# Kernel optimization log

Hardware: AMD Instinct MI355X
Metric: run time of the kernel (lower is better)

Reference implementation:

```python
import jax, jax.numpy as jnp
import numpy as np

BS, L, D, K, G, E = 512, 128, 512, 30, 8, 2048
H = E // 2  # MLP hidden = embed_dim // 2


def setup_inputs():
    key = jax.random.key(0)
    ks = jax.random.split(key, 8)
    features = jax.random.normal(ks[0], (BS, L, D), jnp.float32)
    atten = jax.random.uniform(ks[1], (BS, L, L), jnp.float32)
    rng = np.random.default_rng(0)
    lens = rng.integers(34, L - 1, size=BS)          # caption lengths (>= 34 so lengths-2 > K)
    toks = rng.integers(1, 1000, size=(BS, L))
    pos = np.arange(L)[None, :]
    text = np.where(pos < lens[:, None], toks, 0)    # zero padding
    text[np.arange(BS), lens - 1] = 49407            # eos = max token id -> argmax finds it
    text = jnp.asarray(text, jnp.int32)
    pid = jnp.asarray(np.repeat(np.arange(BS // G), G), jnp.int32)  # 64 groups of size G=8
    dlp_w = jax.random.normal(ks[2], (G, D), jnp.float32)           # weights['weight_8']
    dlp_b = jnp.zeros((G,), jnp.float32)                            # biases['bias_8']
    dlp_lw = jax.random.normal(ks[3], (K * G, E), jnp.float32) * 0.05  # linears['linear_8']
    dlp_lb = jnp.zeros((E,), jnp.float32)
    mlp_w1 = jax.random.normal(ks[4], (D, H), jnp.float32) * 0.04
    mlp_b1 = jnp.zeros((H,), jnp.float32)
    bn_g = jnp.ones((H,), jnp.float32)
    bn_b = jnp.zeros((H,), jnp.float32)
    mlp_w2 = jax.random.normal(ks[5], (H, E), jnp.float32) * 0.03
    mlp_b2 = jnp.zeros((E,), jnp.float32)
    return dict(features=features, atten=atten, text=text, pid=pid,
                dlp_w=dlp_w, dlp_b=dlp_b, dlp_lw=dlp_lw, dlp_lb=dlp_lb,
                mlp_w1=mlp_w1, mlp_b1=mlp_b1, bn_g=bn_g, bn_b=bn_b,
                mlp_w2=mlp_w2, mlp_b2=mlp_b2)


def _l2norm(x, eps=1e-8):
    return x / (jnp.sqrt(jnp.sum(x * x, axis=-1, keepdims=True)) + eps)


def _groups_from_pid(pid_np):
    # replicates the pid_dist==0 grouping + dedup-by-member-set, preserving first-seen order
    groups, order = {}, []
    for i, p in enumerate(pid_np.tolist()):
        if p not in groups:
            groups[p] = []
            order.append(p)
        groups[p].append(i)
    return [groups[p] for p in order]


def reference(features, atten, text, pid, dlp_w, dlp_b, dlp_lw, dlp_lb,
              mlp_w1, mlp_b1, bn_g, bn_b, mlp_w2, mlp_b2):
    bs = features.shape[0]
    b = jnp.arange(bs)
    mask = (text != 0).astype(features.dtype)                  # [bs, L]
    lengths = mask.sum(1) - 2.0                                # [bs]
    eos = jnp.argmax(text, axis=-1)                            # [bs]
    att = atten.at[b, :, eos].set(-1.0).at[:, :, 0].set(-1.0)
    row = att[b, eos, :] * mask                                # [bs, L]
    idx = jax.lax.top_k(row, K)[1]                             # [bs, K] topk token indices
    feats = jnp.take_along_axis(features, idx[:, :, None], axis=1)  # [bs, K, D]

    # pid-based dynamic grouping (host-side; pid is an index input, static)
    glists = _groups_from_pid(np.asarray(pid))
    assert {len(g) for g in glists} == {G}, 'expert params provided for group size G only'
    gi = np.asarray(glists)                                    # [ng, G]
    xg = feats[gi].reshape(gi.shape[0], G * K, D)              # concat group members: [ng, G*K, D]
    # F.linear(x, W[G,D], b).T  ->  [ng, G, G*K]
    h = jnp.einsum('ntd,gd->ngt', xg, dlp_w) + dlp_b[None, :, None]
    yg = h @ dlp_lw + dlp_lb                                   # linear_G: [ng, G, E]
    # scatter-combine each member's row back to its batch position
    new_base = jnp.zeros((bs, E), feats.dtype).at[gi.reshape(-1)].set(yg.reshape(-1, E))
    new_base = _l2norm(new_base)

    # MLP (Linear -> BatchNorm1d(train stats) -> ReLU -> Linear) on l2-normed gathered feats
    x = _l2norm(feats).reshape(bs * K, D) @ mlp_w1 + mlp_b1
    mu, var = x.mean(0), x.var(0)
    x = jax.nn.relu((x - mu) / jnp.sqrt(var + 1e-5) * bn_g + bn_b)
    x = (x @ mlp_w2 + mlp_b2).reshape(bs, K, E)

    # maxk_pool1d_var with pool k=1: per-channel max over first min(length, K) rows
    lens = jnp.minimum(lengths, K).astype(jnp.int32)
    valid = jnp.arange(K)[None, :] < lens[:, None]             # [bs, K]
    pooled = jnp.max(jnp.where(valid[:, :, None], x, -jnp.inf), axis=1)  # [bs, E]
    return (pooled + new_base).astype(jnp.float32)
```

## Files before the change

kernel.cpp:

```cpp
#include <hip/hip_runtime.h>
#include <hip/hip_bf16.h>

#define BS 512
#define LL 128
#define DD 512
#define KK 30
#define GG 8
#define EE 2048
#define HH 1024
#define NROWS (BS*KK)
#define NG (BS/GG)

typedef __attribute__((ext_vector_type(8))) short bf16x8;
typedef __attribute__((ext_vector_type(4))) float f32x4;
typedef __attribute__((address_space(1))) const unsigned int gu32;
typedef __attribute__((address_space(3))) unsigned int lu32;

__device__ __forceinline__ unsigned short f2bf(float f){
  unsigned int x = __float_as_uint(f);
  x = (x + 0x7FFFu + ((x >> 16) & 1u)) >> 16;
  return (unsigned short)x;
}
__device__ __forceinline__ float bf2f(unsigned short u){
  return __uint_as_float(((unsigned int)u) << 16);
}
__device__ __forceinline__ unsigned fkey(float f){
  unsigned b = __float_as_uint(f);
  return (b & 0x80000000u) ? ~b : (b | 0x80000000u);
}
__device__ __forceinline__ float fdec(unsigned k){
  unsigned b = (k & 0x80000000u) ? (k & 0x7FFFFFFFu) : ~k;
  return __uint_as_float(b);
}

#define FENCE asm volatile("" ::: "memory")
#define BARR  do{ FENCE; __builtin_amdgcn_s_barrier(); FENCE; }while(0)
#define LGK0  do{ asm volatile("s_waitcnt lgkmcnt(0)" ::: "memory"); \
                  __builtin_amdgcn_sched_barrier(0); }while(0)
#define VMW(n) asm volatile("s_waitcnt vmcnt(" #n ")" ::: "memory")

__global__ __launch_bounds__(256) void k_pg(const float* __restrict__ atten,
                                            const int* __restrict__ text,
                                            const float* __restrict__ features,
                                            const float* __restrict__ dlp_w,
                                            const float* __restrict__ dlp_b,
                                            const float* __restrict__ w1,
                                            unsigned short* __restrict__ w1t,
                                            unsigned short* __restrict__ nfeats,
                                            float* __restrict__ hval){
  __shared__ int sidx[KK];
  __shared__ float tile[32][33];

  if(blockIdx.x >= BS){
    const int blk = blockIdx.x - BS;
    const int n0 = (blk & 31)*32, k0 = (blk >> 5)*32;
    const int r = threadIdx.x >> 3, c4 = (threadIdx.x & 7)*4;
    const float4 v = *(const float4*)(w1 + (size_t)(k0 + r)*HH + n0 + c4);
    tile[r][c4+0] = v.x; tile[r][c4+1] = v.y; tile[r][c4+2] = v.z; tile[r][c4+3] = v.w;
    __syncthreads();
    ushort4 u;
    u.x = f2bf(tile[c4+0][r]); u.y = f2bf(tile[c4+1][r]);
    u.z = f2bf(tile[c4+2][r]); u.w = f2bf(tile[c4+3][r]);
    *(ushort4*)(w1t + (size_t)(n0 + r)*DD + k0 + c4) = u;
    return;
  }

  const int b = blockIdx.x;
  const int tid = threadIdx.x;
  const int wv = tid >> 6, lane = tid & 63;

  if(wv == 0){
    const int t0 = text[b*LL + lane];
    const int t1 = text[b*LL + 64 + lane];
    int v, vi;
    if(t1 > t0){ v = t1; vi = lane + 64; } else { v = t0; vi = lane; }
#pragma unroll
    for(int off = 32; off; off >>= 1){
      const int ov = __shfl_xor(v, off), oi = __shfl_xor(vi, off);
      if(ov > v || (ov == v && oi < vi)){ v = ov; vi = oi; }
    }
    const int eos = vi;

    const float a0 = atten[(size_t)b*LL*LL + (size_t)eos*LL + lane];
    const float a1 = atten[(size_t)b*LL*LL + (size_t)eos*LL + 64 + lane];
    float r0 = (t0 == 0) ? 0.f : ((lane == 0 || lane == eos) ? -1.f : a0);
    float r1 = (t1 == 0) ? 0.f : ((lane + 64 == eos) ? -1.f : a1);
    for(int k = 0; k < KK; k++){
      float mv; int mi;
      if(r1 > r0){ mv = r1; mi = lane + 64; } else { mv = r0; mi = lane; }
#pragma unroll
      for(int off = 32; off; off >>= 1){
        const float ov = __shfl_xor(mv, off); const int oi = __shfl_xor(mi, off);
        if(ov > mv || (ov == mv && oi < mi)){ mv = ov; mi = oi; }
      }
      if(lane == 0) sidx[k] = mi;
      if(mi == lane)      r0 = -3.f;
      if(mi == lane + 64) r1 = -3.f;
    }
  }
  __syncthreads();

  for(int it = 0; it < 8; it++){
    const int r = it*4 + wv;
    if(r >= KK) break;
    const int l = sidx[r];
    const float4* fp = (const float4*)features + ((size_t)b*LL + l)*(DD/4);
    const float4 v0 = fp[lane], v1 = fp[64 + lane];
    float ss = v0.x*v0.x + v0.y*v0.y + v0.z*v0.z + v0.w*v0.w
             + v1.x*v1.x + v1.y*v1.y + v1.z*v1.z + v1.w*v1.w;
#pragma unroll
    for(int off = 32; off; off >>= 1) ss += __shfl_xor(ss, off);
    float hout = 0.f;
#pragma unroll
    for(int g = 0; g < GG; g++){
      const float4 w0 = ((const float4*)dlp_w)[g*(DD/4) + lane];
      const float4 w1v = ((const float4*)dlp_w)[g*(DD/4) + 64 + lane];
      float hg = v0.x*w0.x + v0.y*w0.y + v0.z*w0.z + v0.w*w0.w
               + v1.x*w1v.x + v1.y*w1v.y + v1.z*w1v.z + v1.w*w1v.w;
#pragma unroll
      for(int off = 32; off; off >>= 1) hg += __shfl_xor(hg, off);
      if(lane == g) hout = hg;
    }
    if(lane < GG) hval[(size_t)(b*KK + r)*GG + lane] = hout + dlp_b[lane];
    const float rn = 1.0f / (sqrtf(ss) + 1e-8f);
    ushort4 u0, u1;
    u0.x = f2bf(v0.x*rn); u0.y = f2bf(v0.y*rn); u0.z = f2bf(v0.z*rn); u0.w = f2bf(v0.w*rn);
    u1.x = f2bf(v1.x*rn); u1.y = f2bf(v1.y*rn); u1.z = f2bf(v1.z*rn); u1.w = f2bf(v1.w*rn);
    ushort4* np = (ushort4*)nfeats + (size_t)(b*KK + r)*(DD/4);
    np[lane] = u0; np[64 + lane] = u1;
  }
}

__global__ __launch_bounds__(256) void k_dlp(const float* __restrict__ hval,
                                             const float* __restrict__ dlp_lw,
                                             const float* __restrict__ dlp_lb,
                                             unsigned short* __restrict__ nbbf,
                                             float* __restrict__ psq2){
  const int et = blockIdx.x;
  const int n  = blockIdx.y;
  const int tid = threadIdx.x;
  __shared__ float hs[GG][GG*KK];
  __shared__ float red[4][4];
  for(int i = tid; i < GG*GG*KK; i += 256){
    const int g = i / (GG*KK), tt = i % (GG*KK);
    const int m = tt / KK, kq = tt % KK;
    hs[g][tt] = hval[(size_t)(((n*GG + m)*KK) + kq)*GG + g];
  }
  __syncthreads();
  const int h = tid >> 7, c = tid & 127;
  const int e = et*128 + c;
  float acc[4] = {0.f, 0.f, 0.f, 0.f};
#pragma unroll 4
  for(int k = 0; k < GG*KK; k++){
    const float w = dlp_lw[(size_t)k*EE + e];
#pragma unroll
    for(int rr = 0; rr < 4; rr++) acc[rr] += hs[h*4 + rr][k] * w;
  }
  const float lb = dlp_lb[e];
  float sq[4];
#pragma unroll
  for(int rr = 0; rr < 4; rr++){
    const float v = acc[rr] + lb;
    nbbf[(size_t)(n*GG + h*4 + rr)*EE + e] = f2bf(v);
    sq[rr] = v*v;
  }
#pragma unroll
  for(int off = 32; off; off >>= 1)
#pragma unroll
    for(int rr = 0; rr < 4; rr++) sq[rr] += __shfl_xor(sq[rr], off);
  const int wv = tid >> 6, lane = tid & 63;
  if(lane == 0){
#pragma unroll
    for(int rr = 0; rr < 4; rr++) red[wv][rr] = sq[rr];
  }
  __syncthreads();
  if(tid < 8){
    const int hh = tid >> 2, rr = tid & 3;
    psq2[(size_t)(n*GG + hh*4 + rr)*16 + et] = red[hh*2][rr] + red[hh*2+1][rr];
  }
}

__global__ __launch_bounds__(256, 2) void k_g1(const unsigned short* __restrict__ A,
                                               const unsigned short* __restrict__ Bt,
                                               const float* __restrict__ bias,
                                               unsigned short* __restrict__ obf,
                                               float* __restrict__ psum,
                                               float* __restrict__ psq){
  const int KD = DD, ND = HH, NBX = HH/128;
  __shared__ short S[2][2][128*64];
  const int tid  = threadIdx.x;
  const int wave = tid >> 6, lane = tid & 63;
  const int wr = wave >> 1, wc = wave & 1;
  const int lrow = lane & 15, kg = lane >> 4;

  const int nwg = gridDim.x, cpx = nwg >> 3;
  const int bid = (blockIdx.x & 7)*cpx + (blockIdx.x >> 3);
  const int bx = bid % NBX, by = bid / NBX;
  const int m0 = by*128, n0 = bx*128;

  const unsigned short* Ab = A  + (size_t)m0*KD;
  const unsigned short* Bb = Bt + (size_t)n0*KD;

#define G1STG(tt, p) { \
  _Pragma("unroll") \
  for(int c = 0; c < 4; c++){ \
    const int i_ = tid + c*256; const int r_ = i_ >> 3; \
    const int g_ = (i_ & 7) ^ (r_ & 7); \
    __builtin_amdgcn_global_load_lds((gu32*)(Ab + (size_t)r_*KD + (tt)*64 + g_*8), \
                                     (lu32*)(&S[p][0][i_*8]), 16, 0, 0); \
  } \
  _Pragma("unroll") \
  for(int c = 0; c < 4; c++){ \
    const int i_ = tid + c*256; const int r_ = i_ >> 3; \
    const int g_ = (i_ & 7) ^ (r_ & 7); \
    __builtin_amdgcn_global_load_lds((gu32*)(Bb + (size_t)r_*KD + (tt)*64 + g_*8), \
                                     (lu32*)(&S[p][1][i_*8]), 16, 0, 0); \
  } \
}

  f32x4 acc[4][4] = {};
  const int NT = KD/64;
  G1STG(0, 0)
  G1STG(1, 1)

  const int arow = wr*64 + lrow;
  const int brow = wc*64 + lrow;
  const int gx0 = (kg       ^ (lrow & 7))*8;
  const int gx1 = ((4 + kg) ^ (lrow & 7))*8;

#pragma unroll 1
  for(int t = 0; t < NT; t++){
    const int p = t & 1;
    if(t < NT-1) VMW(8);
    else         VMW(0);
    BARR;
    const short* Abuf = &S[p][0][0];
    const short* Bbuf = &S[p][1][0];
    bf16x8 af[4], bg[4];
#pragma unroll
    for(int n = 0; n < 4; n++) bg[n] = *(const bf16x8*)(Bbuf + (brow + n*16)*64 + gx0);
#pragma unroll
    for(int m = 0; m < 4; m++) af[m] = *(const bf16x8*)(Abuf + (arow + m*16)*64 + gx0);
    __builtin_amdgcn_s_setprio(1);
#pragma unroll
    for(int m = 0; m < 4; m++)
#pragma unroll
      for(int n = 0; n < 4; n++)
        acc[m][n] = __builtin_amdgcn_mfma_f32_16x16x32_bf16(af[m], bg[n], acc[m][n], 0, 0, 0);
    __builtin_amdgcn_s_setprio(0);
#pragma unroll
    for(int n = 0; n < 4; n++) bg[n] = *(const bf16x8*)(Bbuf + (brow + n*16)*64 + gx1);
#pragma unroll
    for(int m = 0; m < 4; m++) af[m] = *(const bf16x8*)(Abuf + (arow + m*16)*64 + gx1);
    __builtin_amdgcn_s_setprio(1);
#pragma unroll
    for(int m = 0; m < 4; m++)
#pragma unroll
      for(int n = 0; n < 4; n++)
        acc[m][n] = __builtin_amdgcn_mfma_f32_16x16x32_bf16(af[m], bg[n], acc[m][n], 0, 0, 0);
    __builtin_amdgcn_s_setprio(0);
    BARR;
    if(t + 2 < NT){ G1STG(t+2, p) }
  }
#undef G1STG

  const int colb = n0 + wc*64 + lrow;
#pragma unroll
  for(int n = 0; n < 4; n++){
    const float bb = bias[colb + n*16];
    float sv = 0.f, qv = 0.f;
#pragma unroll
    for(int m = 0; m < 4; m++)
#pragma unroll
      for(int r = 0; r < 4; r++){
        const float v = acc[m][n][r] + bb; sv += v; qv += v*v;
      }
    sv += __shfl_xor(sv, 16); sv += __shfl_xor(sv, 32);
    qv += __shfl_xor(qv, 16); qv += __shfl_xor(qv, 32);
    if(lane < 16){
      psum[(size_t)(by*2 + wr)*ND + colb + n*16] = sv;
      psq [(size_t)(by*2 + wr)*ND + colb + n*16] = qv;
    }
#pragma unroll
    for(int m = 0; m < 4; m++){
      const int row = m0 + wr*64 + m*16 + kg*4;
#pragma unroll
      for(int r = 0; r < 4; r++)
        obf[(size_t)(row + r)*ND + colb + n*16] = f2bf(acc[m][n][r] + bb);
    }
  }
}

__global__ __launch_bounds__(256) void k_bnw(const float* __restrict__ psum,
                                             const float* __restrict__ psq,
                                             const float* __restrict__ bn_g,
                                             const float* __restrict__ bn_b,
                                             float* __restrict__ sc,
                                             float* __restrict__ sh,
                                             const float* __restrict__ w2,
                                             unsigned short* __restrict__ w2t){
  if(blockIdx.x < 4){
    const int c = blockIdx.x*256 + threadIdx.x;
    float s = 0.f, q = 0.f;
    for(int i = 0; i < 240; i++){ s += psum[(size_t)i*HH + c]; q += psq[(size_t)i*HH + c]; }
    const float mu  = s * (1.0f/NROWS);
    const float var = q * (1.0f/NROWS) - mu*mu;
    const float sv  = bn_g[c] / sqrtf(var + 1e-5f);
    sc[c] = sv;
    sh[c] = bn_b[c] - mu*sv;
    return;
  }
  __shared__ float tile[32][33];
  const int blk = blockIdx.x - 4;
  const int n0 = (blk & 63)*32, k0 = (blk >> 6)*32;
  const int r = threadIdx.x >> 3, c4 = (threadIdx.x & 7)*4;
  const float4 v = *(const float4*)(w2 + (size_t)(k0 + r)*EE + n0 + c4);
  tile[r][c4+0] = v.x; tile[r][c4+1] = v.y; tile[r][c4+2] = v.z; tile[r][c4+3] = v.w;
  __syncthreads();
  ushort4 u;
  u.x = f2bf(tile[c4+0][r]); u.y = f2bf(tile[c4+1][r]);
  u.z = f2bf(tile[c4+2][r]); u.w = f2bf(tile[c4+3][r]);
  *(ushort4*)(w2t + (size_t)(n0 + r)*HH + k0 + c4) = u;
}

__global__ __launch_bounds__(256) void k_bnrelu(unsigned short* __restrict__ x1,
                                                const float* __restrict__ sc,
                                                const float* __restrict__ sh,
                                                unsigned* __restrict__ pkey){
  const size_t i = (size_t)blockIdx.x*256 + threadIdx.x;
  const int c0 = (int)((i*8) & (HH-1));
  uint4 u = ((uint4*)x1)[i];
  unsigned short* us = (unsigned short*)&u;
  const float4 s0 = *(const float4*)(sc + c0), s1 = *(const float4*)(sc + c0 + 4);
  const float4 h0 = *(const float4*)(sh + c0), h1 = *(const float4*)(sh + c0 + 4);
  const float scv[8] = {s0.x,s0.y,s0.z,s0.w,s1.x,s1.y,s1.z,s1.w};
  const float shv[8] = {h0.x,h0.y,h0.z,h0.w,h1.x,h1.y,h1.z,h1.w};
#pragma unroll
  for(int j = 0; j < 8; j++)
    us[j] = f2bf(fmaxf(bf2f(us[j])*scv[j] + shv[j], 0.f));
  ((uint4*)x1)[i] = u;
  if(blockIdx.x < 1024)
    ((uint4*)pkey)[blockIdx.x*256 + threadIdx.x] =
        make_uint4(0x007FFFFFu, 0x007FFFFFu, 0x007FFFFFu, 0x007FFFFFu);
}

__global__ __launch_bounds__(512, 2) void k_g2(const unsigned short* __restrict__ A,
                                               const unsigned short* __restrict__ Bt,
                                               unsigned* __restrict__ pkey){
  const int KD = HH, ND = EE, NBX = EE/256;
  __shared__ short S[2][2][256*64];
  const int tid  = threadIdx.x;
  const int wave = tid >> 6, lane = tid & 63;
  const int wr = wave >> 2, wc = wave & 3;
  const int lrow = lane & 15, kg = lane >> 4;

  const int nwg = gridDim.x, cpx = nwg >> 3;
  const int bid = (blockIdx.x & 7)*cpx + (blockIdx.x >> 3);
  const int bx = bid % NBX, by = bid / NBX;
  const int m0 = by*256, n0 = bx*256;

  const unsigned short* Ab = A  + (size_t)m0*KD;
  const unsigned short* Bb = Bt + (size_t)n0*KD;

#define STG_A(tt, p, c) { \
  const int i_ = tid + (c)*512; const int r_ = i_ >> 3; \
  const int g_ = (i_ & 7) ^ (r_ & 7); \
  __builtin_amdgcn_global_load_lds((gu32*)(Ab + (size_t)r_*KD + (tt)*64 + g_*8), \
                                   (lu32*)(&S[p][0][i_*8]), 16, 0, 0); }
#define STG_B(tt, p, c) { \
  const int i_ = tid + (c)*512; const int r_ = i_ >> 3; \
  const int g_ = (i_ & 7) ^ (r_ & 7); \
  __builtin_amdgcn_global_load_lds((gu32*)(Bb + (size_t)r_*KD + (tt)*64 + g_*8), \
                                   (lu32*)(&S[p][1][i_*8]), 16, 0, 0); }
#define DSR_B(gx)  _Pragma("unroll") for(int n = 0; n < 4; n++) \
    bg[n] = *(const bf16x8*)(Bbuf + (brow + n*16)*64 + (gx));
#define DSR_AL(gx) _Pragma("unroll") for(int m = 0; m < 4; m++) \
    af[m] = *(const bf16x8*)(Abuf + (arow + m*16)*64 + (gx));
#define DSR_AH(gx) _Pragma("unroll") for(int m = 0; m < 4; m++) \
    af[m] = *(const bf16x8*)(Abuf + (arow + 64 + m*16)*64 + (gx));
#define MFMA_L do{ __builtin_amdgcn_s_setprio(1); \
  _Pragma("unroll") for(int m = 0; m < 4; m++) \
  _Pragma("unroll") for(int n = 0; n < 4; n++) \
    acc[m][n] = __builtin_amdgcn_mfma_f32_16x16x32_bf16(af[m], bg[n], acc[m][n], 0, 0, 0); \
  __builtin_amdgcn_s_setprio(0); }while(0)
#define MFMA_H do{ __builtin_amdgcn_s_setprio(1); \
  _Pragma("unroll") for(int m = 0; m < 4; m++) \
  _Pragma("unroll") for(int n = 0; n < 4; n++) \
    acc[4+m][n] = __builtin_amdgcn_mfma_f32_16x16x32_bf16(af[m], bg[n], acc[4+m][n], 0, 0, 0); \
  __builtin_amdgcn_s_setprio(0); }while(0)

  f32x4 acc[8][4] = {};
  const int NT = KD/64;

  const int arow = wr*128 + lrow;
  const int brow = wc*64  + lrow;
  const int gx0 = (kg       ^ (lrow & 7))*8;
  const int gx1 = ((4 + kg) ^ (lrow & 7))*8;

  STG_A(0, 0, 0) STG_A(0, 0, 2)
  STG_B(0, 0, 0) STG_B(0, 0, 1) STG_B(0, 0, 2) STG_B(0, 0, 3)
  STG_A(0, 0, 1) STG_A(0, 0, 3)
  VMW(2); BARR;

#pragma unroll 1
  for(int t = 0; t < NT-1; t++){
    const int p = t & 1, q = p ^ 1;
    const short* Abuf = &S[p][0][0];
    const short* Bbuf = &S[p][1][0];
    bf16x8 bg[4], af[4];
    DSR_B(gx0); DSR_AL(gx0);
    STG_A(t+1, q, 0) STG_A(t+1, q, 2)
    VMW(2);
    BARR; LGK0;
    MFMA_L;
    BARR;
    DSR_AH(gx0);
    STG_B(t+1, q, 0) STG_B(t+1, q, 1)
    BARR; LGK0;
    MFMA_H;
    BARR;
    DSR_B(gx1); DSR_AL(gx1);
    STG_B(t+1, q, 2) STG_B(t+1, q, 3)
    BARR; LGK0;
    MFMA_L;
    BARR;
    DSR_AH(gx1);
    STG_A(t+1, q, 1) STG_A(t+1, q, 3)
    VMW(2);
    BARR; LGK0;
    MFMA_H;
    BARR;
  }
  {
    const int p = (NT-1) & 1;
    const short* Abuf = &S[p][0][0];
    const short* Bbuf = &S[p][1][0];
    bf16x8 bg[4], af[4];
    DSR_B(gx0); DSR_AL(gx0);
    VMW(0);
    BARR; LGK0;
    MFMA_L;
    BARR;
    DSR_AH(gx0);
    BARR; LGK0;
    MFMA_H;
    BARR;
    DSR_B(gx1); DSR_AL(gx1);
    BARR; LGK0;
    MFMA_L;
    BARR;
    DSR_AH(gx1);
    LGK0;
    MFMA_H;
  }
#undef STG_A
#undef STG_B
#undef DSR_B
#undef DSR_AL
#undef DSR_AH
#undef MFMA_L
#undef MFMA_H

  __syncthreads();
  unsigned* pool = (unsigned*)&S[0][0][0];
  const int b0 = m0 / KK;
  const int b1 = (m0 + 255) / KK;
  const int nseg = b1 - b0 + 1;
  for(int i = tid; i < nseg*256; i += 512) pool[i] = 0x007FFFFFu;
  __syncthreads();
  const int lcol = wc*64 + lrow;
  {
    int cur_b = -1;
    float mx[4];
#pragma unroll
    for(int m = 0; m < 8; m++){
#pragma unroll
      for(int r = 0; r < 4; r++){
        const int row = m0 + wr*128 + m*16 + kg*4 + r;
        const int bt = row / KK;
        if(bt != cur_b){
          if(cur_b >= 0){
#pragma unroll
            for(int n = 0; n < 4; n++)
              atomicMax(&pool[(cur_b - b0)*256 + lcol + n*16], fkey(mx[n]));
          }
          cur_b = bt;
#pragma unroll
          for(int n = 0; n < 4; n++) mx[n] = -INFINITY;
        }
#pragma unroll
        for(int n = 0; n < 4; n++) mx[n] = fmaxf(mx[n], acc[m][n][r]);
      }
    }
#pragma unroll
    for(int n = 0; n < 4; n++)
      atomicMax(&pool[(cur_b - b0)*256 + lcol + n*16], fkey(mx[n]));
  }
  __syncthreads();
  for(int e = tid; e < nseg*256; e += 512){
    const int seg = e >> 8, col = e & 255;
    atomicMax(&pkey[(size_t)(b0 + seg)*ND + n0 + col], pool[e]);
  }
}

__global__ __launch_bounds__(256) void k_final(const unsigned* __restrict__ pkey,
                                               const float* __restrict__ b2,
                                               const unsigned short* __restrict__ nbbf,
                                               const float* __restrict__ psq2,
                                               float* __restrict__ out){
  const size_t i = (size_t)blockIdx.x*256 + threadIdx.x;
  const int c0 = (int)((i*4) & (EE-1));
  const int b = (int)(blockIdx.x >> 1);
  float ssq = 0.f;
#pragma unroll
  for(int j = 0; j < 16; j++) ssq += psq2[(size_t)b*16 + j];
  const float rn = 1.0f / (sqrtf(ssq) + 1e-8f);
  const uint4 k = ((const uint4*)pkey)[i];
  const ushort4 nb4 = ((const ushort4*)nbbf)[i];
  const float4 bb = *(const float4*)(b2 + c0);
  float4 o;
  o.x = fdec(k.x) + bb.x + bf2f(nb4.x)*rn;
  o.y = fdec(k.y) + bb.y + bf2f(nb4.y)*rn;
  o.z = fdec(k.z) + bb.z + bf2f(nb4.z)*rn;
  o.w = fdec(k.w) + bb.w + bf2f(nb4.w)*rn;
  ((float4*)out)[i] = o;
}

extern "C" void kernel_launch(void* const* d_in, const int* in_sizes, int n_in,
                              void* d_out, int out_size, void* d_ws, size_t ws_size,
                              hipStream_t stream){
  const float* features = (const float*)d_in[0];
  const float* atten    = (const float*)d_in[1];
  const int*   text     = (const int*)  d_in[2];
  const float* dlp_w    = (const float*)d_in[4];
  const float* dlp_b    = (const float*)d_in[5];
  const float* dlp_lw   = (const float*)d_in[6];
  const float* dlp_lb   = (const float*)d_in[7];
  const float* w1       = (const float*)d_in[8];
  const float* b1       = (const float*)d_in[9];
  const float* bn_g     = (const float*)d_in[10];
  const float* bn_b     = (const float*)d_in[11];
  const float* w2       = (const float*)d_in[12];
  const float* b2       = (const float*)d_in[13];
  float* out = (float*)d_out;

  char* ws = (char*)d_ws;
  float*          psum   = (float*)(ws + 0);
  float*          psq    = (float*)(ws + 983040);
  unsigned short* w1t    = (unsigned short*)(ws + 1966080);
  float*          hval   = (float*)(ws + 3014656);
  unsigned*       pkey   = (unsigned*)(ws + 0);
  float*          sc     = (float*)(ws + 4196352);
  float*          sh     = (float*)(ws + 4200448);
  float*          psq2   = (float*)(ws + 4204544);
  unsigned short* nfeats = (unsigned short*)(ws + 4237312);
  unsigned short* w2t    = (unsigned short*)(ws + 4237312);
  unsigned short* x1     = (unsigned short*)(ws + 19965952);
  unsigned short* nbbf   = (unsigned short*)(ws + 51423232);

  k_pg<<<BS + 512, 256, 0, stream>>>(atten, text, features, dlp_w, dlp_b,
                                     w1, w1t, nfeats, hval);
  k_dlp<<<dim3(16, NG), 256, 0, stream>>>(hval, dlp_lw, dlp_lb, nbbf, psq2);
  k_g1<<<(HH/128)*(NROWS/128), 256, 0, stream>>>(nfeats, w1t, b1, x1, psum, psq);
  k_bnw<<<4 + 2048, 256, 0, stream>>>(psum, psq, bn_g, bn_b, sc, sh, w2, w2t);
  k_bnrelu<<<(NROWS*HH/8)/256, 256, 0, stream>>>(x1, sc, sh, pkey);
  k_g2<<<(EE/256)*(NROWS/256), 512, 0, stream>>>(x1, w2t, pkey);
  k_final<<<(BS*EE/4)/256, 256, 0, stream>>>(pkey, b2, nbbf, psq2, out);
}
```

Baseline: 177.6 us.

## Fuse DLP linear into first GEMM launch and move W2 transpose earlier

```diff
diff --git a/kernel.cpp b/kernel.cpp
--- a/kernel.cpp
+++ b/kernel.cpp
@@ -46,11 +46,26 @@
                                             const float* __restrict__ dlp_b,
                                             const float* __restrict__ w1,
                                             unsigned short* __restrict__ w1t,
+                                            const float* __restrict__ w2,
+                                            unsigned short* __restrict__ w2t,
                                             unsigned short* __restrict__ nfeats,
                                             float* __restrict__ hval){
   __shared__ int sidx[KK];
   __shared__ float tile[32][33];
 
+  if(blockIdx.x >= BS + 512){
+    const int blk = blockIdx.x - (BS + 512);
+    const int n0 = (blk & 63)*32, k0 = (blk >> 6)*32;
+    const int r = threadIdx.x >> 3, c4 = (threadIdx.x & 7)*4;
+    const float4 v = *(const float4*)(w2 + (size_t)(k0 + r)*EE + n0 + c4);
+    tile[r][c4+0] = v.x; tile[r][c4+1] = v.y; tile[r][c4+2] = v.z; tile[r][c4+3] = v.w;
+    __syncthreads();
+    ushort4 u;
+    u.x = f2bf(tile[c4+0][r]); u.y = f2bf(tile[c4+1][r]);
+    u.z = f2bf(tile[c4+2][r]); u.w = f2bf(tile[c4+3][r]);
+    *(ushort4*)(w2t + (size_t)(n0 + r)*HH + k0 + c4) = u;
+    return;
+  }
   if(blockIdx.x >= BS){
     const int blk = blockIdx.x - BS;
     const int n0 = (blk & 31)*32, k0 = (blk >> 5)*32;
@@ -131,69 +146,74 @@
   }
 }
 
-__global__ __launch_bounds__(256) void k_dlp(const float* __restrict__ hval,
-                                             const float* __restrict__ dlp_lw,
-                                             const float* __restrict__ dlp_lb,
-                                             unsigned short* __restrict__ nbbf,
-                                             float* __restrict__ psq2){
-  const int et = blockIdx.x;
-  const int n  = blockIdx.y;
+__global__ __launch_bounds__(256, 2) void k_dg1(const unsigned short* __restrict__ A,
+                                                const unsigned short* __restrict__ Bt,
+                                                const float* __restrict__ bias,
+                                                unsigned short* __restrict__ obf,
+                                                float* __restrict__ psum,
+                                                float* __restrict__ psq,
+                                                const float* __restrict__ hval,
+                                                const float* __restrict__ dlp_lw,
+                                                const float* __restrict__ dlp_lb,
+                                                unsigned short* __restrict__ nbbf,
+                                                float* __restrict__ psq2){
+  __shared__ char smem[65536];
   const int tid = threadIdx.x;
-  __shared__ float hs[GG][GG*KK];
-  __shared__ float red[4][4];
-  for(int i = tid; i < GG*GG*KK; i += 256){
-    const int g = i / (GG*KK), tt = i % (GG*KK);
-    const int m = tt / KK, kq = tt % KK;
-    hs[g][tt] = hval[(size_t)(((n*GG + m)*KK) + kq)*GG + g];
-  }
-  __syncthreads();
-  const int h = tid >> 7, c = tid & 127;
-  const int e = et*128 + c;
-  float acc[4] = {0.f, 0.f, 0.f, 0.f};
+
+  if(blockIdx.x >= 960){
+    float (*hs)[GG*KK] = (float(*)[GG*KK])smem;
+    float (*red)[4]    = (float(*)[4])(smem + GG*GG*KK*4);
+    const int blk = blockIdx.x - 960;
+    const int et = blk & 15;
+    const int n  = blk >> 4;
+    for(int i = tid; i < GG*GG*KK; i += 256){
+      const int g = i / (GG*KK), tt = i % (GG*KK);
+      const int m = tt / KK, kq = tt % KK;
+      hs[g][tt] = hval[(size_t)(((n*GG + m)*KK) + kq)*GG + g];
+    }
+    __syncthreads();
+    const int h = tid >> 7, c = tid & 127;
+    const int e = et*128 + c;
+    float acc[4] = {0.f, 0.f, 0.f, 0.f};
 #pragma unroll 4
-  for(int k = 0; k < GG*KK; k++){
-    const float w = dlp_lw[(size_t)k*EE + e];
-#pragma unroll
-    for(int rr = 0; rr < 4; rr++) acc[rr] += hs[h*4 + rr][k] * w;
-  }
-  const float lb = dlp_lb[e];
-  float sq[4];
-#pragma unroll
-  for(int rr = 0; rr < 4; rr++){
-    const float v = acc[rr] + lb;
-    nbbf[(size_t)(n*GG + h*4 + rr)*EE + e] = f2bf(v);
-    sq[rr] = v*v;
-  }
-#pragma unroll
-  for(int off = 32; off; off >>= 1)
-#pragma unroll
-    for(int rr = 0; rr < 4; rr++) sq[rr] += __shfl_xor(sq[rr], off);
-  const int wv = tid >> 6, lane = tid & 63;
-  if(lane == 0){
-#pragma unroll
-    for(int rr = 0; rr < 4; rr++) red[wv][rr] = sq[rr];
-  }
-  __syncthreads();
-  if(tid < 8){
-    const int hh = tid >> 2, rr = tid & 3;
-    psq2[(size_t)(n*GG + hh*4 + rr)*16 + et] = red[hh*2][rr] + red[hh*2+1][rr];
-  }
-}
-
-__global__ __launch_bounds__(256, 2) void k_g1(const unsigned short* __restrict__ A,
-                                               const unsigned short* __restrict__ Bt,
-                                               const float* __restrict__ bias,
-                                               unsigned short* __restrict__ obf,
-                                               float* __restrict__ psum,
-                                               float* __restrict__ psq){
+    for(int k = 0; k < GG*KK; k++){
+      const float w = dlp_lw[(size_t)k*EE + e];
+#pragma unroll
+      for(int rr = 0; rr < 4; rr++) acc[rr] += hs[h*4 + rr][k] * w;
+    }
+    const float lb = dlp_lb[e];
+    float sq[4];
+#pragma unroll
+    for(int rr = 0; rr < 4; rr++){
+      const float v = acc[rr] + lb;
+      nbbf[(size_t)(n*GG + h*4 + rr)*EE + e] = f2bf(v);
+      sq[rr] = v*v;
+    }
+#pragma unroll
+    for(int off = 32; off; off >>= 1)
+#pragma unroll
+      for(int rr = 0; rr < 4; rr++) sq[rr] += __shfl_xor(sq[rr], off);
+    const int wv = tid >> 6, lane = tid & 63;
+    if(lane == 0){
+#pragma unroll
+      for(int rr = 0; rr < 4; rr++) red[wv][rr] = sq[rr];
+    }
+    __syncthreads();
+    if(tid < 8){
+      const int hh = tid >> 2, rr = tid & 3;
+      psq2[(size_t)(n*GG + hh*4 + rr)*16 + et] = red[hh*2][rr] + red[hh*2+1][rr];
+    }
+    return;
+  }
+
   const int KD = DD, ND = HH, NBX = HH/128;
-  __shared__ short S[2][2][128*64];
-  const int tid  = threadIdx.x;
+  typedef short lds_t[2][128*64];
+  lds_t* S = (lds_t*)smem;
   const int wave = tid >> 6, lane = tid & 63;
   const int wr = wave >> 1, wc = wave & 1;
   const int lrow = lane & 15, kg = lane >> 4;
 
-  const int nwg = gridDim.x, cpx = nwg >> 3;
+  const int cpx = 960 >> 3;
   const int bid = (blockIdx.x & 7)*cpx + (blockIdx.x >> 3);
   const int bx = bid % NBX, by = bid / NBX;
   const int m0 = by*128, n0 = bx*128;
@@ -554,15 +574,19 @@
   float*          sh     = (float*)(ws + 4200448);
   float*          psq2   = (float*)(ws + 4204544);
   unsigned short* nfeats = (unsigned short*)(ws + 4237312);
-  unsigned short* w2t    = (unsigned short*)(ws + 4237312);
   unsigned short* x1     = (unsigned short*)(ws + 19965952);
   unsigned short* nbbf   = (unsigned short*)(ws + 51423232);
 
-  k_pg<<<BS + 512, 256, 0, stream>>>(atten, text, features, dlp_w, dlp_b,
-                                     w1, w1t, nfeats, hval);
-  k_dlp<<<dim3(16, NG), 256, 0, stream>>>(hval, dlp_lw, dlp_lb, nbbf, psq2);
-  k_g1<<<(HH/128)*(NROWS/128), 256, 0, stream>>>(nfeats, w1t, b1, x1, psum, psq);
-  k_bnw<<<4 + 2048, 256, 0, stream>>>(psum, psq, bn_g, bn_b, sc, sh, w2, w2t);
+  const int sep = (ws_size >= (size_t)53520384 + 4194304) ? 1 : 0;
+  unsigned short* w2t = sep ? (unsigned short*)(ws + 53520384)
+                            : (unsigned short*)(ws + 4237312);
+
+  k_pg<<<BS + 512 + (sep ? 2048 : 0), 256, 0, stream>>>(
+      atten, text, features, dlp_w, dlp_b, w1, w1t, w2, w2t, nfeats, hval);
+  k_dg1<<<960 + 1024, 256, 0, stream>>>(nfeats, w1t, b1, x1, psum, psq,
+                                        hval, dlp_lw, dlp_lb, nbbf, psq2);
+  k_bnw<<<sep ? 4 : (4 + 2048), 256, 0, stream>>>(psum, psq, bn_g, bn_b,
+                                                  sc, sh, w2, w2t);
   k_bnrelu<<<(NROWS*HH/8)/256, 256, 0, stream>>>(x1, sc, sh, pkey);
   k_g2<<<(EE/256)*(NROWS/256), 512, 0, stream>>>(x1, w2t, pkey);
   k_final<<<(BS*EE/4)/256, 256, 0, stream>>>(pkey, b2, nbbf, psq2, out);
```

Result: no change. 180.2 us (+1.5%).
